# Performance work log

Hardware: AMD Instinct MI355X
Metric: run time of the kernel (lower is better)

## Reference

```python
import jax, jax.numpy as jnp
from jax import lax
import numpy as np

SIGMA = 5.0
ALPHA = 50.0
RADIUS = int(4.0 * SIGMA + 0.5)  # scipy gaussian_filter truncate=4.0 -> 20


def _gauss_kernel():
    t = jnp.arange(-RADIUS, RADIUS + 1, dtype=jnp.float32)
    phi = jnp.exp(-0.5 * (t / SIGMA) ** 2)
    return phi / phi.sum()


def _gaussian_blur(f):
    # f: [B, H, W]. scipy mode='reflect' (edge included) == jnp.pad mode='symmetric'.
    k = _gauss_kernel()
    K = 2 * RADIUS + 1
    fp = jnp.pad(f, ((0, 0), (RADIUS, RADIUS), (RADIUS, RADIUS)), mode='symmetric')[:, None]
    z = lax.conv_general_dilated(fp, k.reshape(1, 1, K, 1), (1, 1), 'VALID')
    z = lax.conv_general_dilated(z, k.reshape(1, 1, 1, K), (1, 1), 'VALID')
    return z[:, 0]


def _reflect(i, n):
    # scipy mode='reflect': (d c b a | a b c d | d c b a), period 2n on integer indices
    i = jnp.mod(i, 2 * n)
    return jnp.where(i >= n, 2 * n - 1 - i, i)


def _bilinear(img, yy, xx):
    # img: [H, W]; yy/xx: [H, W] float sample coords (rows, cols)
    H, W = img.shape
    y0 = jnp.floor(yy)
    x0 = jnp.floor(xx)
    wy = yy - y0
    wx = xx - x0
    y0i = y0.astype(jnp.int32)
    x0i = x0.astype(jnp.int32)
    y0r = _reflect(y0i, H)
    y1r = _reflect(y0i + 1, H)
    x0r = _reflect(x0i, W)
    x1r = _reflect(x0i + 1, W)
    v00 = img[y0r, x0r]
    v01 = img[y0r, x1r]
    v10 = img[y1r, x0r]
    v11 = img[y1r, x1r]
    return (v00 * (1 - wy) * (1 - wx) + v01 * (1 - wy) * wx
            + v10 * wy * (1 - wx) + v11 * wy * wx)


def setup_inputs() -> dict:
    key = jax.random.key(0)
    k1, k2, k3 = jax.random.split(key, 3)
    B, H, W = 64, 512, 512
    x = jax.random.normal(k1, (B, 1, H, W), dtype=jnp.float32)
    rand_dx = jax.random.uniform(k2, (B, H, W), dtype=jnp.float32)
    rand_dy = jax.random.uniform(k3, (B, H, W), dtype=jnp.float32)
    return {"x": x, "rand_dx": rand_dx, "rand_dy": rand_dy}


def reference(x, rand_dx, rand_dy):
    # x: [B, 1, H, W]
    B, C, H, W = x.shape
    dx = _gaussian_blur(rand_dx * 2.0 - 1.0) * ALPHA  # [B, H, W]
    dy = _gaussian_blur(rand_dy * 2.0 - 1.0) * ALPHA
    gx, gy = jnp.meshgrid(jnp.arange(W, dtype=x.dtype), jnp.arange(H, dtype=x.dtype))
    yy = gy[None] + dy  # row coords
    xx = gx[None] + dx  # col coords
    warped = jax.vmap(_bilinear)(x[:, 0], yy, xx)  # [B, H, W]
    return warped[:, None]
```

## Files before the change

### kernel.cpp

```cpp
#include <hip/hip_runtime.h>
#include <hip/hip_bf16.h>

#define RADIUS 20
#define KSIZE  41
#define ALPHA_F 50.0f
#define TY     8
#define WID    512
#define HEI    512
#define PW     (WID + 2 * RADIUS)

__device__ constexpr float G[KSIZE] = {
    2.6770e-05f, 5.8390e-05f, 1.22380e-04f, 2.46460e-04f, 4.76840e-04f,
    8.86410e-04f, 1.583160e-03f, 2.716710e-03f, 4.479090e-03f, 7.095210e-03f,
    1.0798630e-02f, 1.5790680e-02f, 2.2185070e-02f, 2.9946720e-02f, 3.8838800e-02f,
    4.8396120e-02f, 5.7940680e-02f, 6.6647650e-02f, 7.3657040e-02f, 7.8211730e-02f,
    7.9791720e-02f,
    7.8211730e-02f, 7.3657040e-02f, 6.6647650e-02f, 5.7940680e-02f, 4.8396120e-02f,
    3.8838800e-02f, 2.9946720e-02f, 2.2185070e-02f, 1.5790680e-02f, 1.0798630e-02f,
    7.095210e-03f, 4.479090e-03f, 2.716710e-03f, 1.583160e-03f, 8.86410e-04f,
    4.76840e-04f, 2.46460e-04f, 1.22380e-04f, 5.8390e-05f, 2.6770e-05f
};

__device__ __forceinline__ int refl(int i, int n) {
    i = (i < 0) ? (-1 - i) : i;
    i = (i >= n) ? (2 * n - 1 - i) : i;
    return i;
}
__device__ __forceinline__ int clampi(int i, int n) {
    return (i < 0) ? 0 : ((i >= n) ? n - 1 : i);
}
__device__ __forceinline__ float h2f(unsigned short h) {
    unsigned int u = ((unsigned int)h) << 16;
    float f;
    __builtin_memcpy(&f, &u, 4);
    return f;
}
__device__ __forceinline__ float ldf(const float* p) { return *p; }
__device__ __forceinline__ float ldf(const __hip_bfloat16* p) { return __bfloat162float(*p); }

template <typename TR, typename TX>
__device__ __forceinline__ void elastic_body(
    const TX* __restrict__ xin, const TR* __restrict__ rdx, const TR* __restrict__ rdy,
    float* __restrict__ outp,
    float (&sdx)[TY][PW], float (&sdy)[TY][PW]) {

    const int tid = threadIdx.x;
    const int y0  = blockIdx.x * TY;
    const int b   = blockIdx.y;
    const size_t base = (size_t)b * (HEI * WID);

    {
        float ax[TY], ay[TY];
        #pragma unroll
        for (int o = 0; o < TY; ++o) { ax[o] = 0.f; ay[o] = 0.f; }

        const TR* px = rdx + base + tid;
        const TR* py = rdy + base + tid;

        #pragma unroll
        for (int r = 0; r < TY + 2 * RADIUS; ++r) {
            const int gy = refl(y0 - RADIUS + r, HEI);
            const float vx = ldf(px + (size_t)gy * WID);
            const float vy = ldf(py + (size_t)gy * WID);
            #pragma unroll
            for (int o = 0; o < TY; ++o) {
                const int t = r - o;
                if (t >= 0 && t < KSIZE) {
                    ax[o] = fmaf(G[t], vx, ax[o]);
                    ay[o] = fmaf(G[t], vy, ay[o]);
                }
            }
        }

        #pragma unroll
        for (int o = 0; o < TY; ++o) {
            const float sx = 2.f * ax[o] - 1.f;
            const float sy = 2.f * ay[o] - 1.f;
            sdx[o][RADIUS + tid] = sx;
            sdy[o][RADIUS + tid] = sy;
            if (tid < RADIUS) {
                sdx[o][RADIUS - 1 - tid] = sx;
                sdy[o][RADIUS - 1 - tid] = sy;
            }
            if (tid >= WID - RADIUS) {
                sdx[o][RADIUS + 2 * WID - 1 - tid] = sx;
                sdy[o][RADIUS + 2 * WID - 1 - tid] = sy;
            }
        }
    }
    __syncthreads();

    const int c4 = tid & 127;
    const int rg = tid >> 7;
    const TX* img = xin + base;

    #pragma unroll
    for (int i = 0; i < 2; ++i) {
        const int o  = rg + 4 * i;
        const int gy = y0 + o;

        float dxv[4] = {0.f, 0.f, 0.f, 0.f};
        float dyv[4] = {0.f, 0.f, 0.f, 0.f};

        {
            float w[44];
            const float4* rp = (const float4*)(&sdx[o][0]);
            #pragma unroll
            for (int q = 0; q < 11; ++q) {
                const float4 v = rp[c4 + q];
                w[4 * q + 0] = v.x; w[4 * q + 1] = v.y;
                w[4 * q + 2] = v.z; w[4 * q + 3] = v.w;
            }
            #pragma unroll
            for (int t = 0; t < KSIZE; ++t) {
                const float g = G[t];
                #pragma unroll
                for (int j = 0; j < 4; ++j) dxv[j] = fmaf(g, w[t + j], dxv[j]);
            }
        }
        {
            float w[44];
            const float4* rp = (const float4*)(&sdy[o][0]);
            #pragma unroll
            for (int q = 0; q < 11; ++q) {
                const float4 v = rp[c4 + q];
                w[4 * q + 0] = v.x; w[4 * q + 1] = v.y;
                w[4 * q + 2] = v.z; w[4 * q + 3] = v.w;
            }
            #pragma unroll
            for (int t = 0; t < KSIZE; ++t) {
                const float g = G[t];
                #pragma unroll
                for (int j = 0; j < 4; ++j) dyv[j] = fmaf(g, w[t + j], dyv[j]);
            }
        }

        float st[4];
        #pragma unroll
        for (int j = 0; j < 4; ++j) {
            const int col = 4 * c4 + j;
            float xx = (float)col + dxv[j] * ALPHA_F;
            float yy = (float)gy  + dyv[j] * ALPHA_F;
            xx = fminf(fmaxf(xx, -2048.f), 2048.f);
            yy = fminf(fmaxf(yy, -2048.f), 2048.f);
            const float x0f = floorf(xx), y0f = floorf(yy);
            const float wx = xx - x0f, wy = yy - y0f;
            const int x0 = (int)x0f, yb = (int)y0f;
            const int x0r = clampi(refl(x0, WID), WID);
            const int x1r = clampi(refl(x0 + 1, WID), WID);
            const int y0r = clampi(refl(yb, HEI), HEI);
            const int y1r = clampi(refl(yb + 1, HEI), HEI);

            const float v00 = ldf(img + (size_t)y0r * WID + x0r);
            const float v01 = ldf(img + (size_t)y0r * WID + x1r);
            const float v10 = ldf(img + (size_t)y1r * WID + x0r);
            const float v11 = ldf(img + (size_t)y1r * WID + x1r);

            st[j] = v00 * (1.f - wy) * (1.f - wx) + v01 * (1.f - wy) * wx
                  + v10 * wy * (1.f - wx) + v11 * wy * wx;
        }

        float4 pack;
        pack.x = st[0]; pack.y = st[1]; pack.z = st[2]; pack.w = st[3];
        *reinterpret_cast<float4*>(outp + base + (size_t)gy * WID + 4 * c4) = pack;
    }
}

__global__ __launch_bounds__(512) void elastic_kernel(
    const void* __restrict__ xin_v, const void* __restrict__ rdx_v,
    const void* __restrict__ rdy_v, float* __restrict__ outp) {

    __shared__ float sdx[TY][PW];
    __shared__ float sdy[TY][PW];
    __shared__ int flags[2];

    const int tid = threadIdx.x;

    if (tid == 0) { flags[0] = 1; flags[1] = 1; }
    __syncthreads();
    {
        const unsigned int wr = ((const unsigned int*)rdx_v)[tid];
        const unsigned int wx = ((const unsigned int*)xin_v)[tid];
        const float r0 = h2f((unsigned short)(wr & 0xffffu));
        const float r1 = h2f((unsigned short)(wr >> 16));
        const float q0 = h2f((unsigned short)(wx & 0xffffu));
        const float q1 = h2f((unsigned short)(wx >> 16));
        const bool rb = (r0 >= 0.f) && (r0 < 1.5f) && (r1 >= 0.f) && (r1 < 1.5f);
        const bool xb = (fabsf(q0) < 32.f) && (fabsf(q1) < 32.f);
        if (!rb) atomicAnd(&flags[0], 0);
        if (!xb) atomicAnd(&flags[1], 0);
    }
    __syncthreads();
    const bool rand_bf = (flags[0] != 0);
    const bool x_bf    = (flags[1] != 0);

    if (rand_bf) {
        if (x_bf) elastic_body<__hip_bfloat16, __hip_bfloat16>(
            (const __hip_bfloat16*)xin_v, (const __hip_bfloat16*)rdx_v,
            (const __hip_bfloat16*)rdy_v, outp, sdx, sdy);
        else elastic_body<__hip_bfloat16, float>(
            (const float*)xin_v, (const __hip_bfloat16*)rdx_v,
            (const __hip_bfloat16*)rdy_v, outp, sdx, sdy);
    } else {
        if (x_bf) elastic_body<float, __hip_bfloat16>(
            (const __hip_bfloat16*)xin_v, (const float*)rdx_v,
            (const float*)rdy_v, outp, sdx, sdy);
        else elastic_body<float, float>(
            (const float*)xin_v, (const float*)rdx_v,
            (const float*)rdy_v, outp, sdx, sdy);
    }
}

extern "C" void kernel_launch(void* const* d_in, const int* in_sizes, int n_in,
                              void* d_out, int out_size, void* d_ws, size_t ws_size,
                              hipStream_t stream) {
    const void* x   = d_in[0];
    const void* rdx = d_in[1];
    const void* rdy = d_in[2];
    float* out = (float*)d_out;

    const int B = in_sizes[1] / (HEI * WID);

    dim3 grid(HEI / TY, B);
    elastic_kernel<<<grid, 512, 0, stream>>>(x, rdx, rdy, out);
    (void)d_ws; (void)ws_size; (void)n_in; (void)out_size;
}
```

Baseline: 342.9 us.

## Drop bf16 runtime dtype detection, remap blocks per XCD, prefetch vertical blur rows

Removes the per-block runtime sniffing of input dtypes and the four templated variants, hard-wiring fp32 inputs. Remaps a 1D grid so each XCD handles whole images (8 images per XCD when B==64), keeping the halo rows and warp source image in that XCD's L2. Adds a register ring buffer that prefetches rows of the vertical blur PF rows ahead to hide load latency. This costs extra registers, and the B==64 specialization only helps that batch size.

```diff
diff --git a/kernel.cpp b/kernel.cpp
--- a/kernel.cpp
+++ b/kernel.cpp
@@ -1,5 +1,4 @@
 #include <hip/hip_runtime.h>
-#include <hip/hip_bf16.h>
 
 #define RADIUS 20
 #define KSIZE  41
@@ -8,6 +7,8 @@
 #define WID    512
 #define HEI    512
 #define PW     (WID + 2 * RADIUS)
+#define NR     (TY + 2 * RADIUS)
+#define PF     8
 
 __device__ constexpr float G[KSIZE] = {
     2.6770e-05f, 5.8390e-05f, 1.22380e-04f, 2.46460e-04f, 4.76840e-04f,
@@ -29,39 +30,57 @@
 __device__ __forceinline__ int clampi(int i, int n) {
     return (i < 0) ? 0 : ((i >= n) ? n - 1 : i);
 }
-__device__ __forceinline__ float h2f(unsigned short h) {
-    unsigned int u = ((unsigned int)h) << 16;
-    float f;
-    __builtin_memcpy(&f, &u, 4);
-    return f;
-}
-__device__ __forceinline__ float ldf(const float* p) { return *p; }
-__device__ __forceinline__ float ldf(const __hip_bfloat16* p) { return __bfloat162float(*p); }
-
-template <typename TR, typename TX>
-__device__ __forceinline__ void elastic_body(
-    const TX* __restrict__ xin, const TR* __restrict__ rdx, const TR* __restrict__ rdy,
-    float* __restrict__ outp,
-    float (&sdx)[TY][PW], float (&sdy)[TY][PW]) {
+
+__global__ __launch_bounds__(512) void elastic_kernel(
+    const float* __restrict__ xin, const float* __restrict__ rdx,
+    const float* __restrict__ rdy, float* __restrict__ outp, int B) {
+
+    __shared__ float sdx[TY][PW];
+    __shared__ float sdy[TY][PW];
 
     const int tid = threadIdx.x;
-    const int y0  = blockIdx.x * TY;
-    const int b   = blockIdx.y;
+
+    int b, band;
+    {
+        const int L = blockIdx.x;
+        if (B == 64) {
+            const int xcd = L & 7;
+            const int s   = L >> 3;
+            b    = xcd * 8 + (s >> 6);
+            band = s & 63;
+        } else {
+            b    = L / (HEI / TY);
+            band = L % (HEI / TY);
+        }
+    }
+    const int y0 = band * TY;
     const size_t base = (size_t)b * (HEI * WID);
 
     {
+        const float* px = rdx + base + tid;
+        const float* py = rdy + base + tid;
+
+        float bx[PF], by[PF];
+        #pragma unroll
+        for (int k = 0; k < PF; ++k) {
+            const int gy = refl(y0 - RADIUS + k, HEI);
+            bx[k] = px[(size_t)gy * WID];
+            by[k] = py[(size_t)gy * WID];
+        }
+
         float ax[TY], ay[TY];
         #pragma unroll
         for (int o = 0; o < TY; ++o) { ax[o] = 0.f; ay[o] = 0.f; }
 
-        const TR* px = rdx + base + tid;
-        const TR* py = rdy + base + tid;
-
-        #pragma unroll
-        for (int r = 0; r < TY + 2 * RADIUS; ++r) {
-            const int gy = refl(y0 - RADIUS + r, HEI);
-            const float vx = ldf(px + (size_t)gy * WID);
-            const float vy = ldf(py + (size_t)gy * WID);
+        #pragma unroll
+        for (int r = 0; r < NR; ++r) {
+            const float vx = bx[r & (PF - 1)];
+            const float vy = by[r & (PF - 1)];
+            if (r + PF < NR) {
+                const int gy = refl(y0 - RADIUS + r + PF, HEI);
+                bx[r & (PF - 1)] = px[(size_t)gy * WID];
+                by[r & (PF - 1)] = py[(size_t)gy * WID];
+            }
             #pragma unroll
             for (int o = 0; o < TY; ++o) {
                 const int t = r - o;
@@ -92,7 +111,7 @@
 
     const int c4 = tid & 127;
     const int rg = tid >> 7;
-    const TX* img = xin + base;
+    const float* img = xin + base;
 
     #pragma unroll
     for (int i = 0; i < 2; ++i) {
@@ -151,10 +170,10 @@
             const int y0r = clampi(refl(yb, HEI), HEI);
             const int y1r = clampi(refl(yb + 1, HEI), HEI);
 
-            const float v00 = ldf(img + (size_t)y0r * WID + x0r);
-            const float v01 = ldf(img + (size_t)y0r * WID + x1r);
-            const float v10 = ldf(img + (size_t)y1r * WID + x0r);
-            const float v11 = ldf(img + (size_t)y1r * WID + x1r);
+            const float v00 = img[(size_t)y0r * WID + x0r];
+            const float v01 = img[(size_t)y0r * WID + x1r];
+            const float v10 = img[(size_t)y1r * WID + x0r];
+            const float v11 = img[(size_t)y1r * WID + x1r];
 
             st[j] = v00 * (1.f - wy) * (1.f - wx) + v01 * (1.f - wy) * wx
                   + v10 * wy * (1.f - wx) + v11 * wy * wx;
@@ -166,62 +185,17 @@
     }
 }
 
-__global__ __launch_bounds__(512) void elastic_kernel(
-    const void* __restrict__ xin_v, const void* __restrict__ rdx_v,
-    const void* __restrict__ rdy_v, float* __restrict__ outp) {
-
-    __shared__ float sdx[TY][PW];
-    __shared__ float sdy[TY][PW];
-    __shared__ int flags[2];
-
-    const int tid = threadIdx.x;
-
-    if (tid == 0) { flags[0] = 1; flags[1] = 1; }
-    __syncthreads();
-    {
-        const unsigned int wr = ((const unsigned int*)rdx_v)[tid];
-        const unsigned int wx = ((const unsigned int*)xin_v)[tid];
-        const float r0 = h2f((unsigned short)(wr & 0xffffu));
-        const float r1 = h2f((unsigned short)(wr >> 16));
-        const float q0 = h2f((unsigned short)(wx & 0xffffu));
-        const float q1 = h2f((unsigned short)(wx >> 16));
-        const bool rb = (r0 >= 0.f) && (r0 < 1.5f) && (r1 >= 0.f) && (r1 < 1.5f);
-        const bool xb = (fabsf(q0) < 32.f) && (fabsf(q1) < 32.f);
-        if (!rb) atomicAnd(&flags[0], 0);
-        if (!xb) atomicAnd(&flags[1], 0);
-    }
-    __syncthreads();
-    const bool rand_bf = (flags[0] != 0);
-    const bool x_bf    = (flags[1] != 0);
-
-    if (rand_bf) {
-        if (x_bf) elastic_body<__hip_bfloat16, __hip_bfloat16>(
-            (const __hip_bfloat16*)xin_v, (const __hip_bfloat16*)rdx_v,
-            (const __hip_bfloat16*)rdy_v, outp, sdx, sdy);
-        else elastic_body<__hip_bfloat16, float>(
-            (const float*)xin_v, (const __hip_bfloat16*)rdx_v,
-            (const __hip_bfloat16*)rdy_v, outp, sdx, sdy);
-    } else {
-        if (x_bf) elastic_body<float, __hip_bfloat16>(
-            (const __hip_bfloat16*)xin_v, (const float*)rdx_v,
-            (const float*)rdy_v, outp, sdx, sdy);
-        else elastic_body<float, float>(
-            (const float*)xin_v, (const float*)rdx_v,
-            (const float*)rdy_v, outp, sdx, sdy);
-    }
-}
-
 extern "C" void kernel_launch(void* const* d_in, const int* in_sizes, int n_in,
                               void* d_out, int out_size, void* d_ws, size_t ws_size,
                               hipStream_t stream) {
-    const void* x   = d_in[0];
-    const void* rdx = d_in[1];
-    const void* rdy = d_in[2];
+    const float* x   = (const float*)d_in[0];
+    const float* rdx = (const float*)d_in[1];
+    const float* rdy = (const float*)d_in[2];
     float* out = (float*)d_out;
 
     const int B = in_sizes[1] / (HEI * WID);
 
-    dim3 grid(HEI / TY, B);
-    elastic_kernel<<<grid, 512, 0, stream>>>(x, rdx, rdy, out);
+    const int nblocks = B * (HEI / TY);
+    elastic_kernel<<<nblocks, 512, 0, stream>>>(x, rdx, rdy, out, B);
     (void)d_ws; (void)ws_size; (void)n_in; (void)out_size;
 }
```

Measured after the change: 283.5 us. 1.21x faster.
